# Kernel tuning notes

Measured on AMD Instinct MI355X. Metric: run time of the kernel, lower is better.

Reference implementation:

```python
import jax, jax.numpy as jnp
import numpy as np

DIM = 1024
N_HEADS = 16
HEAD_DIM = DIM // N_HEADS


def setup_inputs() -> dict:
    key = jax.random.key(0)
    ks = jax.random.split(key, 6)
    s = DIM ** -0.5
    return {
        "x": jax.random.normal(ks[0], (2, 2048, DIM), dtype=jnp.float32),
        "Wq": jax.random.normal(ks[1], (DIM, DIM), dtype=jnp.float32) * s,
        "Wk": jax.random.normal(ks[2], (DIM, DIM), dtype=jnp.float32) * s,
        "Wv": jax.random.normal(ks[3], (DIM, DIM), dtype=jnp.float32) * s,
        "Wo": jax.random.normal(ks[4], (DIM, DIM), dtype=jnp.float32) * s,
        "bo": jax.random.normal(ks[5], (DIM,), dtype=jnp.float32) * 0.01,
    }


def reference(x, Wq, Wk, Wv, Wo, bo):
    B, T, C = x.shape
    H, D = N_HEADS, HEAD_DIM
    # Linear(dim, dim, bias=False): y = x @ W^T
    q = (x @ Wq.T).reshape(B, T, H, D).transpose(0, 2, 1, 3)  # B H T D
    k = (x @ Wk.T).reshape(B, T, H, D).transpose(0, 2, 1, 3)
    v = (x @ Wv.T).reshape(B, T, H, D).transpose(0, 2, 1, 3)
    q = q * (D ** -0.5)
    attn = jnp.einsum('bhqd,bhkd->bhqk', q, k)  # B H T T
    causal_mask = jnp.triu(jnp.ones((T, T), dtype=bool), k=1)
    attn = jnp.where(causal_mask, -jnp.inf, attn)
    attn = jax.nn.softmax(attn, axis=-1)
    out = jnp.einsum('bhqk,bhkd->bhqd', attn, v)  # B H T D
    out = out.transpose(0, 2, 1, 3).reshape(B, T, C)
    return out @ Wo.T + bo
```

## Files before the change

### kernel.cpp

```cpp
#include <hip/hip_runtime.h>
#include <math.h>

typedef __attribute__((ext_vector_type(8))) short bf16x8;
typedef __attribute__((ext_vector_type(4))) float f32x4;

__device__ __forceinline__ ushort f2bf(float f) {
  union { float f; unsigned u; } v; v.f = f;
  return (ushort)((v.u + 0x8000u) >> 16);
}

__device__ __forceinline__ void g2l16(const void* g, void* l) {
  __builtin_amdgcn_global_load_lds((const __attribute__((address_space(1))) unsigned*)g,
                                   (__attribute__((address_space(3))) unsigned*)l, 16, 0, 0);
}

__global__ __launch_bounds__(256) void cast_all(const float* __restrict__ x,
                                                const float* __restrict__ Wq,
                                                const float* __restrict__ Wk,
                                                const float* __restrict__ Wv,
                                                const float* __restrict__ Wo,
                                                ushort* __restrict__ xbf,
                                                ushort* __restrict__ wcat,
                                                float4* __restrict__ O32) {
  int i = blockIdx.x * 256 + threadIdx.x;
  if (i < 1048576) {
    float4 v = ((const float4*)x)[i];
    ushort4 u; u.x = f2bf(v.x); u.y = f2bf(v.y); u.z = f2bf(v.z); u.w = f2bf(v.w);
    ((ushort4*)xbf)[i] = u;
  } else if (i < 2097152) {
    int j = i - 1048576;
    int sel = j >> 18;
    const float* src = (sel == 0) ? Wq : (sel == 1) ? Wk : (sel == 2) ? Wv : Wo;
    float scale = (sel == 0) ? 0.125f * 1.44269504088896f : 1.0f;
    float4 v = ((const float4*)src)[j & 0x3FFFF];
    ushort4 u;
    u.x = f2bf(v.x * scale); u.y = f2bf(v.y * scale);
    u.z = f2bf(v.z * scale); u.w = f2bf(v.w * scale);
    ((ushort4*)wcat)[j] = u;
  } else {
    O32[i - 2097152] = float4{0.f, 0.f, 0.f, 0.f};
  }
}

__global__ __launch_bounds__(256) void gemm_qkv(const ushort* __restrict__ A,
                                                const ushort* __restrict__ B,
                                                ushort* __restrict__ C3,
                                                ushort* __restrict__ Vt) {
  const int K = 1024;
  __shared__ __align__(16) ushort smem[17408];
  ushort* As = smem;
  ushort* Bs = smem + 8192;
  const int m0 = blockIdx.y * 128, n0 = blockIdx.x * 128;
  const int tid = threadIdx.x, lane = tid & 63, wid = tid >> 6;
  const int quad = lane >> 4, lc = lane & 15;
  const int lrow = lane >> 2, lcol = (lane & 3) * 8;
  const int wm = (wid >> 1) * 64, wn = (wid & 1) * 64;

  f32x4 acc[4][4] = {};

  auto stage = [&](int k0, int nb) {
    const ushort* Ag = A + (size_t)(m0 + wid * 32 + lrow) * K + k0 + lcol;
    g2l16(Ag, &As[nb * 4096 + wid * 1024]);
    g2l16(Ag + (size_t)16 * K, &As[nb * 4096 + wid * 1024 + 512]);
    const ushort* Bg = B + (size_t)(n0 + wid * 32 + lrow) * K + k0 + lcol;
    g2l16(Bg, &Bs[nb * 4096 + wid * 1024]);
    g2l16(Bg + (size_t)16 * K, &Bs[nb * 4096 + wid * 1024 + 512]);
  };

  stage(0, 0);
  for (int k0 = 0; k0 < K; k0 += 32) {
    const int nb = (k0 >> 5) & 1;
    __syncthreads();
    if (k0 + 32 < K) stage(k0 + 32, nb ^ 1);

    bf16x8 af[4], bfr[4];
#pragma unroll
    for (int t = 0; t < 4; t++)
      af[t] = *(const bf16x8*)&As[nb * 4096 + (wm + t * 16 + lc) * 32 + quad * 8];
#pragma unroll
    for (int t = 0; t < 4; t++)
      bfr[t] = *(const bf16x8*)&Bs[nb * 4096 + (wn + t * 16 + lc) * 32 + quad * 8];
#pragma unroll
    for (int mt = 0; mt < 4; mt++)
#pragma unroll
      for (int nt = 0; nt < 4; nt++)
        acc[mt][nt] = __builtin_amdgcn_mfma_f32_16x16x32_bf16(af[mt], bfr[nt], acc[mt][nt], 0, 0, 0);
  }

  const int sel = n0 >> 10;
  if (sel < 2) {
#pragma unroll
    for (int mt = 0; mt < 4; mt++) {
#pragma unroll
      for (int r = 0; r < 4; r++) {
        int row = m0 + wm + mt * 16 + quad * 4 + r;
#pragma unroll
        for (int nt = 0; nt < 4; nt++) {
          int col = n0 + wn + nt * 16 + lc;
          size_t dst = ((size_t)sel << 22) + (size_t)row * 1024 + (col & 1023);
          C3[dst] = f2bf(acc[mt][nt][r]);
        }
      }
    }
  } else {
    __syncthreads();
#pragma unroll
    for (int mt = 0; mt < 4; mt++)
#pragma unroll
      for (int r = 0; r < 4; r++) {
        int tl = wm + mt * 16 + quad * 4 + r;
#pragma unroll
        for (int nt = 0; nt < 4; nt++)
          smem[(wn + nt * 16 + lc) * 136 + tl] = f2bf(acc[mt][nt][r]);
      }
    __syncthreads();
    const int hd0 = n0 - 2048, b = m0 >> 11, t_base = m0 & 2047;
#pragma unroll
    for (int i = 0; i < 8; i++) {
      int idx = i * 256 + tid;
      int dl = idx >> 4, tc = (idx & 15) * 8;
      uint4 v = *(const uint4*)&smem[dl * 136 + tc];
      int hd = hd0 + dl;
      *(uint4*)(Vt + (size_t)(b * 16 + (hd >> 6)) * 131072 +
                (size_t)(hd & 63) * 2048 + t_base + tc) = v;
    }
  }
}

__global__ __launch_bounds__(256) void gemm_proj(const ushort* __restrict__ A,
                                                 const ushort* __restrict__ B,
                                                 float* __restrict__ C,
                                                 const float* __restrict__ bias) {
  const int K = 1024;
  __shared__ __align__(16) ushort As[2][2][128 * 32];
  __shared__ __align__(16) ushort Bs[2][2][64 * 32];
  const int m0 = blockIdx.y * 128, n0 = blockIdx.x * 64;
  const int tid = threadIdx.x, lane = tid & 63, wid = tid >> 6;
  const int quad = lane >> 4, lc = lane & 15;
  const int lrow = lane >> 2, lcol = (lane & 3) * 8;
  const int wm = (wid >> 1) * 64, wn = (wid & 1) * 32;

  f32x4 acc[4][2] = {};

  auto stage = [&](int k0, int nb) {
    const ushort* Ag = A + (size_t)(m0 + wid * 32 + lrow) * K + k0 + lcol;
    g2l16(Ag,                       &As[nb][0][wid * 1024]);
    g2l16(Ag + (size_t)16 * K,      &As[nb][0][wid * 1024 + 512]);
    g2l16(Ag + 32,                  &As[nb][1][wid * 1024]);
    g2l16(Ag + (size_t)16 * K + 32, &As[nb][1][wid * 1024 + 512]);
    const ushort* Bg = B + (size_t)(n0 + wid * 16 + lrow) * K + k0 + lcol;
    g2l16(Bg,      &Bs[nb][0][wid * 512]);
    g2l16(Bg + 32, &Bs[nb][1][wid * 512]);
  };

  stage(0, 0);
  for (int k0 = 0; k0 < K; k0 += 64) {
    const int nb = (k0 >> 6) & 1;
    __syncthreads();
    if (k0 + 64 < K) stage(k0 + 64, nb ^ 1);

#pragma unroll
    for (int ks = 0; ks < 2; ks++) {
      bf16x8 af[4], bfr[2];
#pragma unroll
      for (int t = 0; t < 4; t++)
        af[t] = *(const bf16x8*)&As[nb][ks][(wm + t * 16 + lc) * 32 + quad * 8];
#pragma unroll
      for (int t = 0; t < 2; t++)
        bfr[t] = *(const bf16x8*)&Bs[nb][ks][(wn + t * 16 + lc) * 32 + quad * 8];
#pragma unroll
      for (int mt = 0; mt < 4; mt++)
#pragma unroll
        for (int nt = 0; nt < 2; nt++)
          acc[mt][nt] = __builtin_amdgcn_mfma_f32_16x16x32_bf16(af[mt], bfr[nt], acc[mt][nt], 0, 0, 0);
    }
  }

#pragma unroll
  for (int mt = 0; mt < 4; mt++) {
#pragma unroll
    for (int r = 0; r < 4; r++) {
      int row = m0 + wm + mt * 16 + quad * 4 + r;
#pragma unroll
      for (int nt = 0; nt < 2; nt++) {
        int col = n0 + wn + nt * 16 + lc;
        C[(size_t)row * 1024 + col] = acc[mt][nt][r] + bias[col];
      }
    }
  }
}

__global__ __launch_bounds__(256, 3) void attn_kernel(const ushort* __restrict__ Qb,
                                                      const ushort* __restrict__ Kb,
                                                      const ushort* __restrict__ Vt,
                                                      float* __restrict__ O32,
                                                      float* __restrict__ L32) {
  __shared__ __align__(16) ushort Ks[2][2][2048];
  __shared__ __align__(16) ushort Vs[2][2][2048];
  __shared__ __align__(16) ushort Ps[4][32][72];

  const int bh = blockIdx.y, b = bh >> 4, h = bh & 15;
  const int f = (int)blockIdx.x;
  int qi, ci;
  if (f < 16)      { qi = 12 + (f >> 2); ci = f & 3; }
  else if (f < 28) { int g = f - 16; int q3 = g / 3; qi = 8 + q3; ci = g - 3 * q3; }
  else if (f < 36) { int g = f - 28; qi = 4 + (g >> 1); ci = g & 1; }
  else             { qi = f - 36; ci = 0; }
  const int t0 = ci * 8;
  const int t1 = min(t0 + 8, 2 * qi + 2);

  const int tid = threadIdx.x, lane = tid & 63, wid = tid >> 6;
  const int quad = lane >> 4, lc = lane & 15;
  const int lrow = lane >> 2, lcol = (lane & 3) * 8;
  const int qbw = qi * 128 + wid * 32;

  const size_t kbase = (size_t)(b * 2048) * 1024 + h * 64;
  const size_t vbase = (size_t)bh * 131072;

  bf16x8 qf[2][2];
#pragma unroll
  for (int t = 0; t < 2; t++) {
    const ushort* Qp = Qb + kbase + (size_t)(qbw + t * 16 + lc) * 1024;
    qf[t][0] = *(const bf16x8*)(Qp + quad * 8);
    qf[t][1] = *(const bf16x8*)(Qp + 32 + quad * 8);
  }

  bf16x8 ones;
#pragma unroll
  for (int j = 0; j < 8; j++) ones[j] = (short)0x3f80;

  f32x4 o_acc[2][4] = {};
  f32x4 l_acc[2] = {};

  auto stage = [&](int kb, int nb) {
#pragma unroll
    for (int cc = 0; cc < 2; cc++) {
      int ck = wid + cc * 4;
      int half = ck >> 2, rg = ck & 3;
      const ushort* gK = Kb + kbase + (size_t)(kb + rg * 16 + lrow) * 1024 + half * 32 + lcol;
      g2l16(gK, &Ks[nb][half][rg * 512]);
      const ushort* gV = Vt + vbase + (size_t)(rg * 16 + lrow) * 2048 + kb + half * 32 + lcol;
      g2l16(gV, &Vs[nb][half][rg * 512]);
    }
  };

  stage(t0 * 64, 0);
  for (int kt = t0; kt < t1; kt++) {
    const int kb = kt * 64;
    const int nb = (kt - t0) & 1;
    __syncthreads();
    if (kt + 1 < t1) stage(kb + 64, nb ^ 1);

    bf16x8 kf[4][2];
#pragma unroll
    for (int c = 0; c < 4; c++) {
      kf[c][0] = *(const bf16x8*)&Ks[nb][0][(c * 16 + lc) * 32 + quad * 8];
      kf[c][1] = *(const bf16x8*)&Ks[nb][1][(c * 16 + lc) * 32 + quad * 8];
    }

#pragma unroll
    for (int c = 0; c < 4; c++) {
#pragma unroll
      for (int t = 0; t < 2; t++) {
        f32x4 z = {};
        z = __builtin_amdgcn_mfma_f32_16x16x32_bf16(qf[t][0], kf[c][0], z, 0, 0, 0);
        z = __builtin_amdgcn_mfma_f32_16x16x32_bf16(qf[t][1], kf[c][1], z, 0, 0, 0);
        const bool diag = (kb + 63 > qbw + t * 16);
#pragma unroll
        for (int r = 0; r < 4; r++) {
          float sv = z[r];
          if (diag && (kb + c * 16 + lc > qbw + t * 16 + quad * 4 + r)) sv = -1e30f;
          Ps[wid][t * 16 + quad * 4 + r][c * 16 + lc] = f2bf(__builtin_amdgcn_exp2f(sv));
        }
      }
    }
    __asm__ volatile("s_waitcnt lgkmcnt(0)" ::: "memory");
    bf16x8 ap[2][2];
#pragma unroll
    for (int t = 0; t < 2; t++) {
      ap[t][0] = *(const bf16x8*)&Ps[wid][t * 16 + lc][quad * 8];
      ap[t][1] = *(const bf16x8*)&Ps[wid][t * 16 + lc][32 + quad * 8];
    }

#pragma unroll
    for (int t = 0; t < 2; t++) {
      l_acc[t] = __builtin_amdgcn_mfma_f32_16x16x32_bf16(ap[t][0], ones, l_acc[t], 0, 0, 0);
      l_acc[t] = __builtin_amdgcn_mfma_f32_16x16x32_bf16(ap[t][1], ones, l_acc[t], 0, 0, 0);
    }

#pragma unroll
    for (int nt = 0; nt < 4; nt++) {
      bf16x8 vb0 = *(const bf16x8*)&Vs[nb][0][(nt * 16 + lc) * 32 + quad * 8];
      bf16x8 vb1 = *(const bf16x8*)&Vs[nb][1][(nt * 16 + lc) * 32 + quad * 8];
#pragma unroll
      for (int t = 0; t < 2; t++) {
        o_acc[t][nt] = __builtin_amdgcn_mfma_f32_16x16x32_bf16(ap[t][0], vb0, o_acc[t][nt], 0, 0, 0);
        o_acc[t][nt] = __builtin_amdgcn_mfma_f32_16x16x32_bf16(ap[t][1], vb1, o_acc[t][nt], 0, 0, 0);
      }
    }
  }

#pragma unroll
  for (int t = 0; t < 2; t++) {
    if (lc == 0) {
#pragma unroll
      for (int r = 0; r < 4; r++)
        atomicAdd(&L32[(size_t)bh * 2048 + qbw + t * 16 + quad * 4 + r], l_acc[t][r]);
    }
#pragma unroll
    for (int r = 0; r < 4; r++) {
      size_t orow = ((size_t)(b * 2048) + qbw + t * 16 + quad * 4 + r) * 1024 + h * 64 + lc;
#pragma unroll
      for (int nt = 0; nt < 4; nt++)
        atomicAdd(&O32[orow + nt * 16], o_acc[t][nt][r]);
    }
  }
}

__global__ __launch_bounds__(256) void normalize_kernel(const float* __restrict__ O32,
                                                        const float* __restrict__ L32,
                                                        ushort* __restrict__ Out) {
  const int row = blockIdx.x;
  const int tid = threadIdx.x;
  const int col = tid * 4;
  const int b = row >> 11, t = row & 2047, h = col >> 6;
  const float inv = 1.0f / L32[(size_t)(b * 16 + h) * 2048 + t];
  float4 o = ((const float4*)(O32 + (size_t)row * 1024))[tid];
  ushort4 u;
  u.x = f2bf(o.x * inv); u.y = f2bf(o.y * inv);
  u.z = f2bf(o.z * inv); u.w = f2bf(o.w * inv);
  ((ushort4*)(Out + (size_t)row * 1024))[tid] = u;
}

extern "C" void kernel_launch(void* const* d_in, const int* in_sizes, int n_in,
                              void* d_out, int out_size, void* d_ws, size_t ws_size,
                              hipStream_t stream) {
  const float* x  = (const float*)d_in[0];
  const float* Wq = (const float*)d_in[1];
  const float* Wk = (const float*)d_in[2];
  const float* Wv = (const float*)d_in[3];
  const float* Wo = (const float*)d_in[4];
  const float* bo = (const float*)d_in[5];
  float* out = (float*)d_out;

  char* ws = (char*)d_ws;
  ushort* xbf  = (ushort*)(ws);
  ushort* wcat = (ushort*)(ws + (8ull  << 20));
  ushort* qkv  = (ushort*)(ws + (16ull << 20));
  ushort* Qp   = qkv;
  ushort* Kp   = qkv + (1ull << 22);
  ushort* Vt   = qkv + (2ull << 22);
  float*  L32  = (float*)ws;
  float*  O32  = out;
  ushort* attn_out = Qp;

  cast_all<<<12288, 256, 0, stream>>>(x, Wq, Wk, Wv, Wo, xbf, wcat, (float4*)O32);

  gemm_qkv<<<dim3(24, 32), 256, 0, stream>>>(xbf, wcat, qkv, Vt);

  hipMemsetAsync(L32, 0, (size_t)32 * 2048 * 4, stream);

  attn_kernel<<<dim3(40, 32), 256, 0, stream>>>(Qp, Kp, Vt, O32, L32);

  normalize_kernel<<<4096, 256, 0, stream>>>(O32, L32, attn_out);

  gemm_proj<<<dim3(16, 32), 256, 0, stream>>>(
      attn_out, wcat + (size_t)3072 * 1024, out, bo);
}
```

Before: 202.3 us.

## Rework attention with 32x32 MFMA, transposed S, and register-resident P

Rewrites the attention inner loop around 32x32x16 bf16 MFMAs, computing S transposed (K as A operand) so the exponentiated probabilities land in registers already laid out as the A operand of the PV product. This removes the per-wave LDS round trip for P and the ones-vector MFMAs used for row sums, which are now accumulated in registers and combined with a lane shuffle. K/V staging uses an XOR-swizzled LDS layout to cut bank conflicts, fully masked tiles are skipped per wave, and launch bounds are raised to allow four blocks per CU. The risks are higher register pressure under the tighter occupancy bound and correctness of the swizzle and fragment indexing.

```diff
diff --git a/kernel.cpp b/kernel.cpp
--- a/kernel.cpp
+++ b/kernel.cpp
@@ -3,6 +3,7 @@
 
 typedef __attribute__((ext_vector_type(8))) short bf16x8;
 typedef __attribute__((ext_vector_type(4))) float f32x4;
+typedef __attribute__((ext_vector_type(16))) float f32x16;
 
 __device__ __forceinline__ ushort f2bf(float f) {
   union { float f; unsigned u; } v; v.f = f;
@@ -190,14 +191,13 @@
   }
 }
 
-__global__ __launch_bounds__(256, 3) void attn_kernel(const ushort* __restrict__ Qb,
+__global__ __launch_bounds__(256, 4) void attn_kernel(const ushort* __restrict__ Qb,
                                                       const ushort* __restrict__ Kb,
                                                       const ushort* __restrict__ Vt,
                                                       float* __restrict__ O32,
                                                       float* __restrict__ L32) {
-  __shared__ __align__(16) ushort Ks[2][2][2048];
-  __shared__ __align__(16) ushort Vs[2][2][2048];
-  __shared__ __align__(16) ushort Ps[4][32][72];
+  __shared__ __align__(16) ushort Ks[2][4096];
+  __shared__ __align__(16) ushort Vs[2][4096];
 
   const int bh = blockIdx.y, b = bh >> 4, h = bh & 15;
   const int f = (int)blockIdx.x;
@@ -210,39 +210,37 @@
   const int t1 = min(t0 + 8, 2 * qi + 2);
 
   const int tid = threadIdx.x, lane = tid & 63, wid = tid >> 6;
-  const int quad = lane >> 4, lc = lane & 15;
-  const int lrow = lane >> 2, lcol = (lane & 3) * 8;
+  const int hi = lane >> 5, ln = lane & 31;
   const int qbw = qi * 128 + wid * 32;
+  const int qg = qbw + ln;
 
   const size_t kbase = (size_t)(b * 2048) * 1024 + h * 64;
   const size_t vbase = (size_t)bh * 131072;
 
-  bf16x8 qf[2][2];
-#pragma unroll
-  for (int t = 0; t < 2; t++) {
-    const ushort* Qp = Qb + kbase + (size_t)(qbw + t * 16 + lc) * 1024;
-    qf[t][0] = *(const bf16x8*)(Qp + quad * 8);
-    qf[t][1] = *(const bf16x8*)(Qp + 32 + quad * 8);
-  }
-
-  bf16x8 ones;
-#pragma unroll
-  for (int j = 0; j < 8; j++) ones[j] = (short)0x3f80;
-
-  f32x4 o_acc[2][4] = {};
-  f32x4 l_acc[2] = {};
+  bf16x8 qf[4];
+  {
+    const ushort* Qp = Qb + kbase + (size_t)qg * 1024 + hi * 8;
+#pragma unroll
+    for (int dc = 0; dc < 4; dc++)
+      qf[dc] = *(const bf16x8*)(Qp + dc * 16);
+  }
+
+  f32x16 o_acc[2] = {};
+  float l_own = 0.f;
+
+  const int krow = lane >> 3, kcol = lane & 7;
+  const int dsw = (kcol ^ krow) << 3;
 
   auto stage = [&](int kb, int nb) {
-#pragma unroll
-    for (int cc = 0; cc < 2; cc++) {
-      int ck = wid + cc * 4;
-      int half = ck >> 2, rg = ck & 3;
-      const ushort* gK = Kb + kbase + (size_t)(kb + rg * 16 + lrow) * 1024 + half * 32 + lcol;
-      g2l16(gK, &Ks[nb][half][rg * 512]);
-      const ushort* gV = Vt + vbase + (size_t)(rg * 16 + lrow) * 2048 + kb + half * 32 + lcol;
-      g2l16(gV, &Vs[nb][half][rg * 512]);
-    }
+    const ushort* gK = Kb + kbase + (size_t)(kb + wid * 8 + krow) * 1024 + dsw;
+    g2l16(gK, &Ks[nb][wid * 512]);
+    g2l16(gK + (size_t)32 * 1024, &Ks[nb][2048 + wid * 512]);
+    const ushort* gV = Vt + vbase + (size_t)(wid * 8 + krow) * 2048 + kb + dsw;
+    g2l16(gV, &Vs[nb][wid * 512]);
+    g2l16(gV + (size_t)32 * 2048, &Vs[nb][2048 + wid * 512]);
   };
+
+  const int sx = ln & 7;
 
   stage(t0 * 64, 0);
   for (int kt = t0; kt < t1; kt++) {
@@ -250,70 +248,79 @@
     const int nb = (kt - t0) & 1;
     __syncthreads();
     if (kt + 1 < t1) stage(kb + 64, nb ^ 1);
-
-    bf16x8 kf[4][2];
-#pragma unroll
-    for (int c = 0; c < 4; c++) {
-      kf[c][0] = *(const bf16x8*)&Ks[nb][0][(c * 16 + lc) * 32 + quad * 8];
-      kf[c][1] = *(const bf16x8*)&Ks[nb][1][(c * 16 + lc) * 32 + quad * 8];
-    }
-
-#pragma unroll
-    for (int c = 0; c < 4; c++) {
-#pragma unroll
-      for (int t = 0; t < 2; t++) {
-        f32x4 z = {};
-        z = __builtin_amdgcn_mfma_f32_16x16x32_bf16(qf[t][0], kf[c][0], z, 0, 0, 0);
-        z = __builtin_amdgcn_mfma_f32_16x16x32_bf16(qf[t][1], kf[c][1], z, 0, 0, 0);
-        const bool diag = (kb + 63 > qbw + t * 16);
-#pragma unroll
-        for (int r = 0; r < 4; r++) {
-          float sv = z[r];
-          if (diag && (kb + c * 16 + lc > qbw + t * 16 + quad * 4 + r)) sv = -1e30f;
-          Ps[wid][t * 16 + quad * 4 + r][c * 16 + lc] = f2bf(__builtin_amdgcn_exp2f(sv));
+    if (kb > qbw + 31) continue;
+
+    const ushort* ks = &Ks[nb][0];
+    const ushort* vs = &Vs[nb][0];
+
+    unsigned pa[4][4];
+#pragma unroll
+    for (int g64 = 0; g64 < 2; g64++) {
+      f32x16 s;
+#pragma unroll
+      for (int z = 0; z < 16; z++) s[z] = 0.f;
+#pragma unroll
+      for (int dc = 0; dc < 4; dc++) {
+        bf16x8 kf = *(const bf16x8*)&ks[(g64 * 32 + ln) * 64 + (((dc * 2 + hi) ^ sx) << 3)];
+        s = __builtin_amdgcn_mfma_f32_32x32x16_bf16(kf, qf[dc], s, 0, 0, 0);
+      }
+      const bool dmask = (kb + g64 * 32 + 31 > qbw);
+      unsigned U[8];
+#pragma unroll
+      for (int g = 0; g < 4; g++) {
+        float e[4];
+#pragma unroll
+        for (int j = 0; j < 4; j++) {
+          float sv = s[g * 4 + j];
+          if (dmask && (kb + g64 * 32 + g * 8 + hi * 4 + j > qg)) sv = -1e30f;
+          e[j] = __builtin_amdgcn_exp2f(sv);
         }
-      }
-    }
-    __asm__ volatile("s_waitcnt lgkmcnt(0)" ::: "memory");
-    bf16x8 ap[2][2];
-#pragma unroll
-    for (int t = 0; t < 2; t++) {
-      ap[t][0] = *(const bf16x8*)&Ps[wid][t * 16 + lc][quad * 8];
-      ap[t][1] = *(const bf16x8*)&Ps[wid][t * 16 + lc][32 + quad * 8];
-    }
-
-#pragma unroll
-    for (int t = 0; t < 2; t++) {
-      l_acc[t] = __builtin_amdgcn_mfma_f32_16x16x32_bf16(ap[t][0], ones, l_acc[t], 0, 0, 0);
-      l_acc[t] = __builtin_amdgcn_mfma_f32_16x16x32_bf16(ap[t][1], ones, l_acc[t], 0, 0, 0);
-    }
-
-#pragma unroll
-    for (int nt = 0; nt < 4; nt++) {
-      bf16x8 vb0 = *(const bf16x8*)&Vs[nb][0][(nt * 16 + lc) * 32 + quad * 8];
-      bf16x8 vb1 = *(const bf16x8*)&Vs[nb][1][(nt * 16 + lc) * 32 + quad * 8];
-#pragma unroll
-      for (int t = 0; t < 2; t++) {
-        o_acc[t][nt] = __builtin_amdgcn_mfma_f32_16x16x32_bf16(ap[t][0], vb0, o_acc[t][nt], 0, 0, 0);
-        o_acc[t][nt] = __builtin_amdgcn_mfma_f32_16x16x32_bf16(ap[t][1], vb1, o_acc[t][nt], 0, 0, 0);
-      }
-    }
-  }
-
-#pragma unroll
-  for (int t = 0; t < 2; t++) {
-    if (lc == 0) {
-#pragma unroll
-      for (int r = 0; r < 4; r++)
-        atomicAdd(&L32[(size_t)bh * 2048 + qbw + t * 16 + quad * 4 + r], l_acc[t][r]);
-    }
-#pragma unroll
-    for (int r = 0; r < 4; r++) {
-      size_t orow = ((size_t)(b * 2048) + qbw + t * 16 + quad * 4 + r) * 1024 + h * 64 + lc;
-#pragma unroll
-      for (int nt = 0; nt < 4; nt++)
-        atomicAdd(&O32[orow + nt * 16], o_acc[t][nt][r]);
-    }
+        ushort b0 = f2bf(e[0]), b1 = f2bf(e[1]), b2 = f2bf(e[2]), b3 = f2bf(e[3]);
+        U[g * 2]     = (unsigned)b0 | ((unsigned)b1 << 16);
+        U[g * 2 + 1] = (unsigned)b2 | ((unsigned)b3 << 16);
+      }
+#pragma unroll
+      for (int t = 0; t < 8; t++) {
+        union { unsigned u; float f; } plo, phi;
+        plo.u = U[t] << 16;
+        phi.u = U[t] & 0xffff0000u;
+        l_own += plo.f + phi.f;
+      }
+#pragma unroll
+      for (int half = 0; half < 2; half++)
+#pragma unroll
+        for (int w = 0; w < 4; w++)
+          pa[g64 * 2 + half][w] = U[half * 4 + w];
+    }
+
+#pragma unroll
+    for (int m = 0; m < 4; m++) {
+      bf16x8 pfrag;
+#pragma unroll
+      for (int w = 0; w < 4; w++) ((unsigned*)&pfrag)[w] = pa[m][w];
+#pragma unroll
+      for (int dg = 0; dg < 2; dg++) {
+        const ushort* vrow = &vs[(dg * 32 + ln) * 64];
+        bf16x8 vbf;
+        *(unsigned long long*)&vbf =
+            *(const unsigned long long*)&vrow[(((2 * m) ^ sx) << 3) + 4 * hi];
+        *((unsigned long long*)&vbf + 1) =
+            *(const unsigned long long*)&vrow[(((2 * m + 1) ^ sx) << 3) + 4 * hi];
+        o_acc[dg] = __builtin_amdgcn_mfma_f32_32x32x16_bf16(pfrag, vbf, o_acc[dg], 0, 0, 0);
+      }
+    }
+  }
+
+  {
+    float lt = l_own + __shfl_xor(l_own, 32);
+    if (hi == 0) atomicAdd(&L32[(size_t)bh * 2048 + qg], lt);
+  }
+#pragma unroll
+  for (int r = 0; r < 16; r++) {
+    int q = qbw + (r & 3) + ((r >> 2) << 3) + hi * 4;
+    size_t orow = ((size_t)(b * 2048) + q) * 1024 + h * 64 + ln;
+    atomicAdd(&O32[orow], o_acc[0][r]);
+    atomicAdd(&O32[orow + 32], o_acc[1][r]);
   }
 }
 
```

Measured after the change: 200.8 us. Within noise of the previous version (-0.8%).
